# Performance work log

Measured on AMD Instinct MI355X. Metric: run time of the kernel, lower is better.

The kernel has to match this reference:

```python
import jax, jax.numpy as jnp
import numpy as np

B, N, H = 32, 1024, 512
DT = 0.1  # euler step size = t[1]-t[0] for torchdiffeq euler on t=[0.0,0.1]

def setup_inputs() -> dict:
    key = jax.random.key(0)
    ks = jax.random.split(key, 8)
    s = 1.0 / np.sqrt(2 * H)
    return {
        "inp": jax.random.normal(ks[0], (B, N, H), jnp.float32),
        "hz": jax.random.normal(ks[1], (B, N, H), jnp.float32),
        # func1: tanh(Linear(2H -> 2H)) ODE dynamics
        "Wf": jax.random.uniform(ks[2], (2 * H, 2 * H), jnp.float32, -s, s),
        "bf": jnp.zeros((2 * H,), jnp.float32),
        # mlp head: Linear(2H,2H) -> ReLU -> Linear(2H,H) -> Tanh
        "W1": jax.random.uniform(ks[3], (2 * H, 2 * H), jnp.float32, -s, s),
        "b1": jnp.zeros((2 * H,), jnp.float32),
        "W2": jax.random.uniform(ks[4], (2 * H, H), jnp.float32, -s, s),
        "b2": jnp.zeros((H,), jnp.float32),
    }

def reference(inp, hz, Wf, bf, W1, b1, W2, b2):
    # h0 = cat([input, hz], -1)  -> [B, N, 2H]
    h = jnp.concatenate([inp, hz], axis=-1)
    def func1(h):  # dh/dt (time-independent dynamics)
        return jnp.tanh(h @ Wf + bf)
    # two odeint calls, each a single fixed euler step over t=[0.0, 0.1]
    for _ in range(2):
        h = h + DT * func1(h)
    # MLP head
    h = jax.nn.relu(h @ W1 + b1)
    h = jnp.tanh(h @ W2 + b2)
    return h  # [B, N, H]
```

## Files before the change

### kernel.cpp

```cpp
#include <hip/hip_runtime.h>
#include <hip/hip_bf16.h>

typedef __attribute__((ext_vector_type(8))) short short8;
typedef __attribute__((ext_vector_type(4))) float floatx4;

__device__ __forceinline__ ushort f2bf(float x) {
    __hip_bfloat16 h = __float2bfloat16(x);
    return __builtin_bit_cast(ushort, h);
}
__device__ __forceinline__ float bf2f(ushort u) {
    __hip_bfloat16 h = __builtin_bit_cast(__hip_bfloat16, u);
    return __bfloat162float(h);
}

__device__ __forceinline__ float fast_tanh(float z) {
    float e = __expf(2.0f * z);
    return 1.0f - 2.0f * __builtin_amdgcn_rcpf(e + 1.0f);
}

__device__ __forceinline__ void gload_lds16(const ushort* g, ushort* l) {
    __builtin_amdgcn_global_load_lds(
        (const __attribute__((address_space(1))) unsigned int*)(const void*)g,
        (__attribute__((address_space(3))) unsigned int*)(void*)l,
        16, 0, 0);
}

__global__ void prep(const float* __restrict__ inp, const float* __restrict__ hz,
                     const float* __restrict__ Wf, const float* __restrict__ W1,
                     const float* __restrict__ W2,
                     ushort* __restrict__ h0, ushort* __restrict__ WfT,
                     ushort* __restrict__ W1T, ushort* __restrict__ W2T) {
    int bid = blockIdx.x;
    int tid = threadIdx.x;
    __shared__ float tile[32][33];
    if (bid < 32768) {
        const float* src = (bid < 16384) ? inp : hz;
        int half = (bid < 16384) ? 0 : 1;
        int b = bid - half * 16384;
        size_t i = ((size_t)b * 256 + tid) * 4;
        size_t row = i >> 9;
        int col = (int)(i & 511);
        float4 v = *(const float4*)(src + i);
        ushort4 o = make_ushort4(f2bf(v.x), f2bf(v.y), f2bf(v.z), f2bf(v.w));
        *(ushort4*)(h0 + row * 1024 + half * 512 + col) = o;
    } else {
        int t = bid - 32768;
        const float* W;
        ushort* WT;
        int K = 1024, N = 1024;
        if (t < 1024)      { W = Wf; WT = WfT; }
        else if (t < 2048) { W = W1; WT = W1T; t -= 1024; }
        else               { W = W2; WT = W2T; t -= 2048; N = 512; }
        int tx = tid & 31, ty = tid >> 5;
        int nb = (t % (N / 32)) * 32, kb = (t / (N / 32)) * 32;
        #pragma unroll
        for (int j = ty; j < 32; j += 8)
            tile[j][tx] = W[(size_t)(kb + j) * N + nb + tx];
        __syncthreads();
        #pragma unroll
        for (int j = ty; j < 32; j += 8)
            WT[(size_t)(nb + j) * K + kb + tx] = f2bf(tile[tx][j]);
    }
}

template <int MODE, int NOUT, int NX>
__global__ __launch_bounds__(512, 4) void gemm_ep(
    const ushort* __restrict__ A, const ushort* __restrict__ BT,
    const float* __restrict__ bias,
    ushort* __restrict__ outB, float* __restrict__ outF) {
    constexpr int K = 1024;
    __shared__ ushort As[128 * 32];
    __shared__ ushort Bs[256 * 32];

    const int tid = threadIdx.x;
    const int wave = tid >> 6, lane = tid & 63;

    const int id = blockIdx.x;
    const int inner = id >> 3;
    const int nTile = inner % NX;
    const int mTile = (id & 7) * 32 + inner / NX;
    const int mBase = mTile * 128;
    const int nBase = nTile * 256;
    const int waveM = wave >> 2;
    const int waveN = wave & 3;

    const int ca = wave * 64 + lane;
    const int ra = ca >> 2;
    const int qa = (ca & 3) ^ ((ra >> 1) & 3);
    const ushort* agA = A + (size_t)(mBase + ra) * K + qa * 8;
    const ushort* bg0 = BT + (size_t)(nBase + ra) * K + qa * 8;
    const ushort* bg1 = BT + (size_t)(nBase + ra + 128) * K + qa * 8;
    ushort* asD  = As + (size_t)(wave * 64) * 8;
    ushort* bsD0 = Bs + (size_t)(wave * 64) * 8;
    ushort* bsD1 = Bs + (size_t)(wave * 64 + 512) * 8;

    floatx4 acc[4][4];
    #pragma unroll
    for (int i = 0; i < 4; i++)
        #pragma unroll
        for (int j = 0; j < 4; j++) acc[i][j] = (floatx4)(0.f);

    const int mrow = lane & 15;
    const int g = lane >> 4;
    const int pq = g ^ ((mrow >> 1) & 3);
    const int kqOff = pq * 8;

    for (int k0 = 0; k0 < K; k0 += 32) {
        gload_lds16(agA + k0, asD);
        gload_lds16(bg0 + k0, bsD0);
        gload_lds16(bg1 + k0, bsD1);
        __syncthreads();

        short8 af[4], bfr[4];
        #pragma unroll
        for (int t = 0; t < 4; t++) {
            af[t]  = *(const short8*)(As + (waveM * 64 + t * 16 + mrow) * 32 + kqOff);
            bfr[t] = *(const short8*)(Bs + (waveN * 64 + t * 16 + mrow) * 32 + kqOff);
        }
        #pragma unroll
        for (int mt = 0; mt < 4; mt++)
            #pragma unroll
            for (int nt = 0; nt < 4; nt++)
                acc[mt][nt] = __builtin_amdgcn_mfma_f32_16x16x32_bf16(
                    af[mt], bfr[nt], acc[mt][nt], 0, 0, 0);
        __syncthreads();
    }

    const int col0 = nBase + waveN * 64 + (lane & 15);
    const int row0 = mBase + waveM * 64 + (lane >> 4) * 4;
    #pragma unroll
    for (int mt = 0; mt < 4; mt++) {
        #pragma unroll
        for (int nt = 0; nt < 4; nt++) {
            const int col = col0 + nt * 16;
            const float bv = bias[col];
            #pragma unroll
            for (int r = 0; r < 4; r++) {
                const int row = row0 + mt * 16 + r;
                const float z = acc[mt][nt][r] + bv;
                if (MODE == 1) {
                    float carry = bf2f(A[(size_t)row * K + col]);
                    outB[(size_t)row * NOUT + col] = f2bf(carry + 0.1f * fast_tanh(z));
                } else if (MODE == 2) {
                    outB[(size_t)row * NOUT + col] = f2bf(fmaxf(z, 0.f));
                } else {
                    outF[(size_t)row * NOUT + col] = fast_tanh(z);
                }
            }
        }
    }
}

extern "C" void kernel_launch(void* const* d_in, const int* in_sizes, int n_in,
                              void* d_out, int out_size, void* d_ws, size_t ws_size,
                              hipStream_t stream) {
    const float* inp = (const float*)d_in[0];
    const float* hz  = (const float*)d_in[1];
    const float* Wf  = (const float*)d_in[2];
    const float* bf_ = (const float*)d_in[3];
    const float* W1  = (const float*)d_in[4];
    const float* b1  = (const float*)d_in[5];
    const float* W2  = (const float*)d_in[6];
    const float* b2  = (const float*)d_in[7];
    float* out = (float*)d_out;

    char* ws = (char*)d_ws;
    ushort* WfT  = (ushort*)(ws);
    ushort* W1T  = (ushort*)(ws + (size_t)(2 << 20));
    ushort* W2T  = (ushort*)(ws + (size_t)(4 << 20));
    ushort* bufA = (ushort*)(ws + (size_t)(8 << 20));
    ushort* bufB = (ushort*)(ws + (size_t)(8 << 20) + ((size_t)64 << 20));

    prep<<<35328, 256, 0, stream>>>(inp, hz, Wf, W1, W2, bufA, WfT, W1T, W2T);

    gemm_ep<1, 1024, 4><<<1024, 512, 0, stream>>>(bufA, WfT, bf_, bufB, nullptr);
    gemm_ep<1, 1024, 4><<<1024, 512, 0, stream>>>(bufB, WfT, bf_, bufA, nullptr);
    gemm_ep<2, 1024, 4><<<1024, 512, 0, stream>>>(bufA, W1T, b1, bufB, nullptr);
    gemm_ep<3, 512, 2><<<512, 512, 0, stream>>>(bufB, W2T, b2, nullptr, out);
}
```

Baseline: 456.8 us.

## Fuse prep and four GEMM launches into one persistent cooperative kernel

Replaces the separate prep kernel and four GEMM launches with a single cooperative persistent kernel. The kernel converts the inputs, transposes the weights, then runs the four GEMM phases with grid-wide syncs between them. Tiles are looped over with a grid-stride schedule sized from occupancy. This aims to remove launch overhead and tail gaps between kernels. In exchange it adds grid-sync cost, and the block count is capped by occupancy, which may leave tile counts unbalanced across blocks. The prep work also now runs as grid-stride loops rather than as many small blocks.

```diff
diff --git a/kernel.cpp b/kernel.cpp
--- a/kernel.cpp
+++ b/kernel.cpp
@@ -1,5 +1,8 @@
 #include <hip/hip_runtime.h>
 #include <hip/hip_bf16.h>
+#include <hip/hip_cooperative_groups.h>
+
+namespace cg = cooperative_groups;
 
 typedef __attribute__((ext_vector_type(8))) short short8;
 typedef __attribute__((ext_vector_type(4))) float floatx4;
@@ -25,130 +28,147 @@
         16, 0, 0);
 }
 
-__global__ void prep(const float* __restrict__ inp, const float* __restrict__ hz,
-                     const float* __restrict__ Wf, const float* __restrict__ W1,
-                     const float* __restrict__ W2,
-                     ushort* __restrict__ h0, ushort* __restrict__ WfT,
-                     ushort* __restrict__ W1T, ushort* __restrict__ W2T) {
-    int bid = blockIdx.x;
-    int tid = threadIdx.x;
-    __shared__ float tile[32][33];
-    if (bid < 32768) {
-        const float* src = (bid < 16384) ? inp : hz;
-        int half = (bid < 16384) ? 0 : 1;
-        int b = bid - half * 16384;
-        size_t i = ((size_t)b * 256 + tid) * 4;
-        size_t row = i >> 9;
-        int col = (int)(i & 511);
-        float4 v = *(const float4*)(src + i);
-        ushort4 o = make_ushort4(f2bf(v.x), f2bf(v.y), f2bf(v.z), f2bf(v.w));
-        *(ushort4*)(h0 + row * 1024 + half * 512 + col) = o;
-    } else {
-        int t = bid - 32768;
-        const float* W;
-        ushort* WT;
-        int K = 1024, N = 1024;
-        if (t < 1024)      { W = Wf; WT = WfT; }
-        else if (t < 2048) { W = W1; WT = W1T; t -= 1024; }
-        else               { W = W2; WT = W2T; t -= 2048; N = 512; }
-        int tx = tid & 31, ty = tid >> 5;
-        int nb = (t % (N / 32)) * 32, kb = (t / (N / 32)) * 32;
-        #pragma unroll
-        for (int j = ty; j < 32; j += 8)
-            tile[j][tx] = W[(size_t)(kb + j) * N + nb + tx];
-        __syncthreads();
-        #pragma unroll
-        for (int j = ty; j < 32; j += 8)
-            WT[(size_t)(nb + j) * K + kb + tx] = f2bf(tile[tx][j]);
-    }
-}
-
 template <int MODE, int NOUT, int NX>
-__global__ __launch_bounds__(512, 4) void gemm_ep(
+__device__ __forceinline__ void gemm_phase(
     const ushort* __restrict__ A, const ushort* __restrict__ BT,
     const float* __restrict__ bias,
-    ushort* __restrict__ outB, float* __restrict__ outF) {
+    ushort* __restrict__ outB, float* __restrict__ outF,
+    int nTiles, ushort* As, ushort* Bs) {
     constexpr int K = 1024;
-    __shared__ ushort As[128 * 32];
-    __shared__ ushort Bs[256 * 32];
-
     const int tid = threadIdx.x;
     const int wave = tid >> 6, lane = tid & 63;
-
-    const int id = blockIdx.x;
-    const int inner = id >> 3;
-    const int nTile = inner % NX;
-    const int mTile = (id & 7) * 32 + inner / NX;
-    const int mBase = mTile * 128;
-    const int nBase = nTile * 256;
     const int waveM = wave >> 2;
     const int waveN = wave & 3;
 
     const int ca = wave * 64 + lane;
     const int ra = ca >> 2;
     const int qa = (ca & 3) ^ ((ra >> 1) & 3);
-    const ushort* agA = A + (size_t)(mBase + ra) * K + qa * 8;
-    const ushort* bg0 = BT + (size_t)(nBase + ra) * K + qa * 8;
-    const ushort* bg1 = BT + (size_t)(nBase + ra + 128) * K + qa * 8;
     ushort* asD  = As + (size_t)(wave * 64) * 8;
     ushort* bsD0 = Bs + (size_t)(wave * 64) * 8;
     ushort* bsD1 = Bs + (size_t)(wave * 64 + 512) * 8;
-
-    floatx4 acc[4][4];
-    #pragma unroll
-    for (int i = 0; i < 4; i++)
-        #pragma unroll
-        for (int j = 0; j < 4; j++) acc[i][j] = (floatx4)(0.f);
 
     const int mrow = lane & 15;
     const int g = lane >> 4;
     const int pq = g ^ ((mrow >> 1) & 3);
     const int kqOff = pq * 8;
 
-    for (int k0 = 0; k0 < K; k0 += 32) {
-        gload_lds16(agA + k0, asD);
-        gload_lds16(bg0 + k0, bsD0);
-        gload_lds16(bg1 + k0, bsD1);
-        __syncthreads();
-
-        short8 af[4], bfr[4];
+    for (int id = blockIdx.x; id < nTiles; id += gridDim.x) {
+        const int inner = id >> 3;
+        const int nTile = inner % NX;
+        const int mTile = (id & 7) * 32 + inner / NX;
+        const int mBase = mTile * 128;
+        const int nBase = nTile * 256;
+
+        const ushort* agA = A + (size_t)(mBase + ra) * K + qa * 8;
+        const ushort* bg0 = BT + (size_t)(nBase + ra) * K + qa * 8;
+        const ushort* bg1 = BT + (size_t)(nBase + ra + 128) * K + qa * 8;
+
+        floatx4 acc[4][4];
         #pragma unroll
-        for (int t = 0; t < 4; t++) {
-            af[t]  = *(const short8*)(As + (waveM * 64 + t * 16 + mrow) * 32 + kqOff);
-            bfr[t] = *(const short8*)(Bs + (waveN * 64 + t * 16 + mrow) * 32 + kqOff);
+        for (int i = 0; i < 4; i++)
+            #pragma unroll
+            for (int j = 0; j < 4; j++) acc[i][j] = (floatx4)(0.f);
+
+        for (int k0 = 0; k0 < K; k0 += 32) {
+            gload_lds16(agA + k0, asD);
+            gload_lds16(bg0 + k0, bsD0);
+            gload_lds16(bg1 + k0, bsD1);
+            __syncthreads();
+
+            short8 af[4], bfr[4];
+            #pragma unroll
+            for (int t = 0; t < 4; t++) {
+                af[t]  = *(const short8*)(As + (waveM * 64 + t * 16 + mrow) * 32 + kqOff);
+                bfr[t] = *(const short8*)(Bs + (waveN * 64 + t * 16 + mrow) * 32 + kqOff);
+            }
+            #pragma unroll
+            for (int mt = 0; mt < 4; mt++)
+                #pragma unroll
+                for (int nt = 0; nt < 4; nt++)
+                    acc[mt][nt] = __builtin_amdgcn_mfma_f32_16x16x32_bf16(
+                        af[mt], bfr[nt], acc[mt][nt], 0, 0, 0);
+            __syncthreads();
         }
+
+        const int col0 = nBase + waveN * 64 + (lane & 15);
+        const int row0 = mBase + waveM * 64 + (lane >> 4) * 4;
         #pragma unroll
-        for (int mt = 0; mt < 4; mt++)
-            #pragma unroll
-            for (int nt = 0; nt < 4; nt++)
-                acc[mt][nt] = __builtin_amdgcn_mfma_f32_16x16x32_bf16(
-                    af[mt], bfr[nt], acc[mt][nt], 0, 0, 0);
-        __syncthreads();
-    }
-
-    const int col0 = nBase + waveN * 64 + (lane & 15);
-    const int row0 = mBase + waveM * 64 + (lane >> 4) * 4;
-    #pragma unroll
-    for (int mt = 0; mt < 4; mt++) {
-        #pragma unroll
-        for (int nt = 0; nt < 4; nt++) {
-            const int col = col0 + nt * 16;
-            const float bv = bias[col];
-            #pragma unroll
-            for (int r = 0; r < 4; r++) {
-                const int row = row0 + mt * 16 + r;
-                const float z = acc[mt][nt][r] + bv;
-                if (MODE == 1) {
-                    float carry = bf2f(A[(size_t)row * K + col]);
-                    outB[(size_t)row * NOUT + col] = f2bf(carry + 0.1f * fast_tanh(z));
-                } else if (MODE == 2) {
-                    outB[(size_t)row * NOUT + col] = f2bf(fmaxf(z, 0.f));
-                } else {
-                    outF[(size_t)row * NOUT + col] = fast_tanh(z);
+        for (int mt = 0; mt < 4; mt++) {
+            #pragma unroll
+            for (int nt = 0; nt < 4; nt++) {
+                const int col = col0 + nt * 16;
+                const float bv = bias[col];
+                #pragma unroll
+                for (int r = 0; r < 4; r++) {
+                    const int row = row0 + mt * 16 + r;
+                    const float z = acc[mt][nt][r] + bv;
+                    if (MODE == 1) {
+                        float carry = bf2f(A[(size_t)row * K + col]);
+                        outB[(size_t)row * NOUT + col] = f2bf(carry + 0.1f * fast_tanh(z));
+                    } else if (MODE == 2) {
+                        outB[(size_t)row * NOUT + col] = f2bf(fmaxf(z, 0.f));
+                    } else {
+                        outF[(size_t)row * NOUT + col] = fast_tanh(z);
+                    }
                 }
             }
         }
     }
+}
+
+__global__ __launch_bounds__(512, 4) void fused(
+    const float* __restrict__ inp, const float* __restrict__ hz,
+    const float* __restrict__ Wf, const float* __restrict__ bff,
+    const float* __restrict__ W1, const float* __restrict__ b1,
+    const float* __restrict__ W2, const float* __restrict__ b2,
+    ushort* __restrict__ bufA, ushort* __restrict__ bufB,
+    ushort* __restrict__ WfT, ushort* __restrict__ W1T,
+    ushort* __restrict__ W2T, float* __restrict__ out) {
+    __shared__ ushort As[128 * 32];
+    __shared__ ushort Bs[256 * 32];
+
+    cg::grid_group grid = cg::this_grid();
+    const int tid = threadIdx.x;
+    const int nthr = gridDim.x * 512;
+
+    for (int i = blockIdx.x * 512 + tid; i < 32768 * 256; i += nthr) {
+        size_t row = (size_t)(i >> 8);
+        int col = (i & 255) * 4;
+        float4 v = (col < 512) ? *(const float4*)(inp + row * 512 + col)
+                               : *(const float4*)(hz + row * 512 + (col - 512));
+        ushort4 o = make_ushort4(f2bf(v.x), f2bf(v.y), f2bf(v.z), f2bf(v.w));
+        *(ushort4*)(bufA + row * 1024 + col) = o;
+    }
+    {
+        float* tp = (float*)Bs + (tid >> 8) * 1056;
+        const int stid = tid & 255;
+        const int tx = stid & 31, ty = stid >> 5;
+        for (int t = blockIdx.x; t < 1280; t += gridDim.x) {
+            int t2 = t * 2 + (tid >> 8);
+            const float* W; ushort* WT; int N = 1024;
+            if (t2 < 1024)      { W = Wf; WT = WfT; }
+            else if (t2 < 2048) { W = W1; WT = W1T; t2 -= 1024; }
+            else                { W = W2; WT = W2T; t2 -= 2048; N = 512; }
+            int nb = (t2 % (N / 32)) * 32, kb = (t2 / (N / 32)) * 32;
+            #pragma unroll
+            for (int j = ty; j < 32; j += 8)
+                tp[j * 33 + tx] = W[(size_t)(kb + j) * N + nb + tx];
+            __syncthreads();
+            #pragma unroll
+            for (int j = ty; j < 32; j += 8)
+                WT[(size_t)(nb + j) * 1024 + kb + tx] = f2bf(tp[tx * 33 + j]);
+            __syncthreads();
+        }
+    }
+
+    __threadfence(); grid.sync(); __threadfence();
+    gemm_phase<1, 1024, 4>(bufA, WfT, bff, bufB, nullptr, 1024, As, Bs);
+    __threadfence(); grid.sync(); __threadfence();
+    gemm_phase<1, 1024, 4>(bufB, WfT, bff, bufA, nullptr, 1024, As, Bs);
+    __threadfence(); grid.sync(); __threadfence();
+    gemm_phase<2, 1024, 4>(bufA, W1T, b1, bufB, nullptr, 1024, As, Bs);
+    __threadfence(); grid.sync(); __threadfence();
+    gemm_phase<3, 512, 2>(bufB, W2T, b2, nullptr, out, 512, As, Bs);
 }
 
 extern "C" void kernel_launch(void* const* d_in, const int* in_sizes, int n_in,
@@ -171,10 +191,16 @@
     ushort* bufA = (ushort*)(ws + (size_t)(8 << 20));
     ushort* bufB = (ushort*)(ws + (size_t)(8 << 20) + ((size_t)64 << 20));
 
-    prep<<<35328, 256, 0, stream>>>(inp, hz, Wf, W1, W2, bufA, WfT, W1T, W2T);
-
-    gemm_ep<1, 1024, 4><<<1024, 512, 0, stream>>>(bufA, WfT, bf_, bufB, nullptr);
-    gemm_ep<1, 1024, 4><<<1024, 512, 0, stream>>>(bufB, WfT, bf_, bufA, nullptr);
-    gemm_ep<2, 1024, 4><<<1024, 512, 0, stream>>>(bufA, W1T, b1, bufB, nullptr);
-    gemm_ep<3, 512, 2><<<512, 512, 0, stream>>>(bufB, W2T, b2, nullptr, out);
-}
+    int maxB = 0;
+    if (hipOccupancyMaxActiveBlocksPerMultiprocessor(&maxB, fused, 512, 0) != hipSuccess
+        || maxB < 1)
+        maxB = 1;
+    int nB = maxB * 256;
+    if (nB > 1024) nB = 1024;
+
+    void* args[] = {(void*)&inp, (void*)&hz, (void*)&Wf, (void*)&bf_,
+                    (void*)&W1, (void*)&b1, (void*)&W2, (void*)&b2,
+                    (void*)&bufA, (void*)&bufB, (void*)&WfT, (void*)&W1T,
+                    (void*)&W2T, (void*)&out};
+    hipLaunchCooperativeKernel((void*)fused, dim3(nB), dim3(512), args, 0, stream);
+}
```

Result: slower. 1.115 ms (+144.1%).
